# Optimization experiments

Hardware: AMD Instinct MI355X
Metric: run time of the kernel (lower is better)

The kernel has to match this reference:

```python
import jax, jax.numpy as jnp
import numpy as np

NUM_HEADS = 8
DIM = 256
NUM_Q = 1


def setup_inputs() -> dict:
    key = jax.random.key(0)
    ks = jax.random.split(key, 10)
    B, H, W, C = 4, 56, 56, DIM
    mask_h = mask_w = 7
    WinNum = mask_h * mask_w
    x = jax.random.normal(ks[0], (B, H, W, C), dtype=jnp.float32)
    clstoken = jax.random.normal(ks[1], (B, NUM_Q, C), dtype=jnp.float32)
    mask = jax.random.bernoulli(ks[2], 0.3, (B, WinNum, WinNum))
    # ensure each window attends to itself (avoid fully-masked rows)
    eye = jnp.eye(WinNum, dtype=bool)[None]
    mask = jnp.logical_or(mask, eye)
    Wqkv = jax.random.normal(ks[3], (C, 3 * C), dtype=jnp.float32) * (C ** -0.5)
    bqkv = jnp.zeros((3 * C,), dtype=jnp.float32)
    Wo = jax.random.normal(ks[4], (C, C), dtype=jnp.float32) * (C ** -0.5)
    bo = jnp.zeros((C,), dtype=jnp.float32)
    lepe_k = jax.random.normal(ks[5], (3, 3, 1, C), dtype=jnp.float32) * 0.1  # depthwise HWIO
    lepe_b = jnp.zeros((C,), dtype=jnp.float32)
    return {"x": x, "clstoken": clstoken, "mask": mask, "mask_h": mask_h,
            "mask_w": mask_w, "Wqkv": Wqkv, "bqkv": bqkv, "Wo": Wo, "bo": bo,
            "lepe_k": lepe_k, "lepe_b": lepe_b}


def _forward(x, clstoken, mask, mask_h, mask_w, Wqkv, bqkv, Wo, bo, lepe_k, lepe_b):
    B, H, W, C = x.shape
    num_q = clstoken.shape[1]
    Nh = NUM_HEADS
    Hd = C // Nh
    Win_h, Win_w = H // mask_h, W // mask_w
    WinPix = Win_h * Win_w
    WinNum = mask_h * mask_w
    L_win = H * W
    scale = C ** -0.5

    qkv = x @ Wqkv + bqkv                       # [B,H,W,3C]
    q, k, v = jnp.split(qkv, 3, axis=-1)
    qkv_cls = clstoken @ Wqkv + bqkv            # [B,Q,3C]
    q_cls, k_cls, v_cls = jnp.split(qkv_cls, 3, axis=-1)

    # depthwise lepe conv on v (NHWC)
    lepe = jax.lax.conv_general_dilated(
        v, lepe_k, window_strides=(1, 1), padding='SAME',
        dimension_numbers=('NHWC', 'HWIO', 'NHWC'), feature_group_count=C) + lepe_b

    def to_win(t):  # b (j h)(i w)(Nh Hd) -> b Nh (j i h w) Hd
        t = t.reshape(B, mask_h, Win_h, mask_w, Win_w, Nh, Hd)
        t = t.transpose(0, 5, 1, 3, 2, 4, 6)
        return t.reshape(B, Nh, L_win, Hd)

    def cls_heads(t):  # b q (Nh Hd) -> b Nh q Hd
        return t.reshape(B, num_q, Nh, Hd).transpose(0, 2, 1, 3)

    q_all = jnp.concatenate([to_win(q), cls_heads(q_cls)], axis=2)
    k_all = jnp.concatenate([to_win(k), cls_heads(k_cls)], axis=2)
    v_all = jnp.concatenate([to_win(v), cls_heads(v_cls)], axis=2)

    # token-level block mask; cls block (id WinNum) is globally visible
    blk = jnp.concatenate([jnp.arange(L_win) // WinPix,
                           jnp.full((num_q,), WinNum)])
    mask_ext = jnp.pad(mask, ((0, 0), (0, 1), (0, 1)), constant_values=True)
    tok_mask = mask_ext[:, blk[:, None], blk[None, :]]  # [B,L,L]

    scores = jnp.einsum('bnqd,bnkd->bnqk', q_all, k_all) * scale
    neg = jnp.finfo(scores.dtype).min
    scores = jnp.where(tok_mask[:, None], scores, neg)
    attn = jax.nn.softmax(scores, axis=-1)
    out = jnp.einsum('bnqk,bnkd->bnqd', attn, v_all)   # [B,Nh,L,Hd]

    cls_out = out[:, :, -num_q:, :]
    x_out = out[:, :, :-num_q, :]
    # b Nh (j i h w) Hd -> b (j h)(i w)(Nh Hd)
    x_out = x_out.reshape(B, Nh, mask_h, mask_w, Win_h, Win_w, Hd)
    x_out = x_out.transpose(0, 2, 4, 3, 5, 1, 6).reshape(B, H, W, C)
    cls_out = cls_out.transpose(0, 2, 1, 3).reshape(B, num_q, C)

    x_out = (x_out + lepe) @ Wo + bo
    cls_out = cls_out @ Wo + bo
    return x_out, cls_out


def reference(x, clstoken, mask, mask_h, mask_w, Wqkv, bqkv, Wo, bo, lepe_k, lepe_b):
    return _forward(x, clstoken, mask, mask_h, mask_w, Wqkv, bqkv, Wo, bo, lepe_k, lepe_b)
```

## Files before the change

kernel.cpp:

```cpp
#include <hip/hip_runtime.h>
#include <math.h>

#define B_      4
#define NH      8
#define HD      32
#define WINNUM  49
#define LWIN    3136
#define NTOK    3137
#define NPIX    12544
#define MROWS   12548
#define SCALE_L2E 0.09016844005556021f

typedef _Float16 half_t;
using half8  = __attribute__((ext_vector_type(8))) half_t;
using half4  = __attribute__((ext_vector_type(4))) half_t;
using f32x4  = __attribute__((ext_vector_type(4))) float;
using f32x16 = __attribute__((ext_vector_type(16))) float;

__device__ __forceinline__ float fexp2(float x) {
    return __builtin_amdgcn_exp2f(x);
}
__device__ __forceinline__ unsigned pack2(float a, float b) {
    auto h = __builtin_amdgcn_cvt_pkrtz(a, b);
    return __builtin_bit_cast(unsigned, h);
}
__device__ __forceinline__ half8 as_h8(int4 v) {
    return __builtin_bit_cast(half8, v);
}
__device__ __forceinline__ unsigned short h2u(half_t h) {
    return __builtin_bit_cast(unsigned short, h);
}

__global__ __launch_bounds__(256)
void prep(const float* __restrict__ Wqkv, const float* __restrict__ Wo,
          half_t* __restrict__ Wqkvt, half_t* __restrict__ Wot)
{
    const int idx = blockIdx.x * 256 + threadIdx.x;
    const int stride = gridDim.x * 256;
    for (int i = idx; i < 768 * 256; i += stride) {
        int n = i >> 8, k = i & 255;
        Wqkvt[i] = (half_t)Wqkv[k * 768 + n];
    }
    for (int i = idx; i < 256 * 256; i += stride) {
        int n = i >> 8, k = i & 255;
        Wot[i] = (half_t)Wo[k * 256 + n];
    }
}

__global__ __launch_bounds__(256, 1)
void qkv_gemm(const float* __restrict__ x, const float* __restrict__ cls,
              const half_t* __restrict__ Bt, const float* __restrict__ bqkv,
              half_t* __restrict__ qh, half_t* __restrict__ kh,
              half_t* __restrict__ khcls, half_t* __restrict__ vh,
              half_t* __restrict__ vplain)
{
    __shared__ __align__(16) char smem[40960];
    short (*As)[128 * 40] = (short (*)[128 * 40])smem;
    short (*Bs)[128 * 40] = (short (*)[128 * 40])(smem + 20480);
    half_t* Cl = (half_t*)smem;

    const int m0 = blockIdx.y * 128, n0 = blockIdx.x * 128;
    const int tid = threadIdx.x;
    const int lane = tid & 63, wv = tid >> 6;
    const int wm = wv >> 1, wn = wv & 1;
    const int qi = lane & 15, g = lane >> 4;
    f32x4 acc[4][4] = {};

    float4 rfa[2][2];
    int4 rb[2];
    auto issue = [&](int k0) {
#pragma unroll
        for (int i = 0; i < 2; ++i) {
            int ch = tid + 256 * i;
            int row = ch >> 2, kc = (ch & 3) * 8;
            int m = m0 + row;
            if (m < MROWS) {
                const float* src = ((m < NPIX) ? (x + (size_t)m * 256)
                                               : (cls + (size_t)(m - NPIX) * 256)) + k0 + kc;
                rfa[i][0] = *(const float4*)src;
                rfa[i][1] = *(const float4*)(src + 4);
            } else {
                rfa[i][0] = rfa[i][1] = make_float4(0.f, 0.f, 0.f, 0.f);
            }
            rb[i] = *(const int4*)(Bt + (size_t)(n0 + row) * 256 + k0 + kc);
        }
    };
    auto commit = [&](int bu) {
#pragma unroll
        for (int i = 0; i < 2; ++i) {
            int ch = tid + 256 * i;
            int row = ch >> 2, kc = (ch & 3) * 8;
            uint4 pa = make_uint4(pack2(rfa[i][0].x, rfa[i][0].y), pack2(rfa[i][0].z, rfa[i][0].w),
                                  pack2(rfa[i][1].x, rfa[i][1].y), pack2(rfa[i][1].z, rfa[i][1].w));
            *(uint4*)&As[bu][row * 40 + kc] = pa;
            *(int4*)&Bs[bu][row * 40 + kc] = rb[i];
        }
    };

    issue(0); commit(0);
    __syncthreads();
    int buf = 0;
    for (int s = 0; s < 8; ++s) {
        if (s < 7) issue((s + 1) * 32);
        half8 af[4], bf[4];
#pragma unroll
        for (int f = 0; f < 4; ++f) {
            af[f] = *(const half8*)&As[buf][(wm * 64 + f * 16 + qi) * 40 + g * 8];
            bf[f] = *(const half8*)&Bs[buf][(wn * 64 + f * 16 + qi) * 40 + g * 8];
        }
#pragma unroll
        for (int fm = 0; fm < 4; ++fm)
#pragma unroll
            for (int fn = 0; fn < 4; ++fn)
                acc[fm][fn] = __builtin_amdgcn_mfma_f32_16x16x32_f16(af[fm], bf[fn], acc[fm][fn], 0, 0, 0);
        if (s < 7) commit(buf ^ 1);
        __syncthreads();
        buf ^= 1;
    }

    const int part = n0 >> 8;
    const int headbase = (n0 & 255) >> 5;

    float bq[4];
#pragma unroll
    for (int fn = 0; fn < 4; ++fn) bq[fn] = bqkv[n0 + wn * 64 + fn * 16 + qi];
#pragma unroll
    for (int fm = 0; fm < 4; ++fm)
#pragma unroll
        for (int r = 0; r < 4; ++r) {
            int rl = wm * 64 + fm * 16 + g * 4 + r;
#pragma unroll
            for (int fn = 0; fn < 4; ++fn) {
                float val = acc[fm][fn][r] + bq[fn];
                if (part == 0) val *= SCALE_L2E;
                Cl[rl * 136 + wn * 64 + fn * 16 + qi] = (half_t)val;
            }
        }
    __syncthreads();

    if (part == 0 || part == 2) {
        half_t* base = (part == 0) ? qh : vplain;
#pragma unroll
        for (int c = 0; c < 2; ++c) {
            int ch = tid + 256 * c;
            int row = ch >> 2, hd4 = ch & 3;
            int m = m0 + row;
            if (m >= MROWS) continue;
            int b, tok;
            if (m < NPIX) {
                b = m / LWIN;
                int p = m - b * LWIN;
                int hh = p / 56, ww = p - hh * 56;
                tok = ((hh >> 3) * 7 + (ww >> 3)) * 64 + ((hh & 7) << 3) + (ww & 7);
            } else { b = m - NPIX; tok = LWIN; }
            size_t bh = (size_t)(b * NH + headbase + hd4);
            const half_t* src = Cl + row * 136 + hd4 * 32;
            half_t* dst = base + (bh * NTOK + tok) * 32;
#pragma unroll
            for (int j = 0; j < 4; ++j)
                *(int4*)(dst + j * 8) = *(const int4*)(src + j * 8);
        }
    }
    if (part == 1) {
#pragma unroll
        for (int c = 0; c < 2; ++c) {
            int ch = tid + 256 * c;
            int row = ch >> 2, hd4 = ch & 3;
            int m = m0 + row;
            if (m >= MROWS) continue;
            size_t bh;
            half_t* dst;
            if (m < NPIX) {
                int b = m / LWIN;
                int p = m - b * LWIN;
                int hh = p / 56, ww = p - hh * 56;
                int tok = ((hh >> 3) * 7 + (ww >> 3)) * 64 + ((hh & 7) << 3) + (ww & 7);
                bh = (size_t)(b * NH + headbase + hd4);
                dst = kh + bh * (WINNUM * 2560) + (tok >> 6) * 2560 + (tok & 63) * 40;
            } else {
                bh = (size_t)((m - NPIX) * NH + headbase + hd4);
                dst = khcls + bh * 32;
            }
            const half_t* src = Cl + row * 136 + hd4 * 32;
#pragma unroll
            for (int j = 0; j < 4; ++j)
                *(int4*)(dst + j * 8) = *(const int4*)(src + j * 8);
        }
    }
    if (part == 2) {
#pragma unroll
        for (int c = 0; c < 8; ++c) {
            int ch = tid + 256 * c;
            int run = ch >> 7;
            int hd4 = (ch >> 5) & 3;
            int d   = ch & 31;
            int m = m0 + run * 8;
            if (m >= NPIX) continue;
            int b = m / LWIN;
            int p = m - b * LWIN;
            int hh = p / 56, ww = p - hh * 56;
            int win = (hh >> 3) * 7 + (ww >> 3);
            int tokb = (hh & 7) << 3;
            const half_t* src = Cl + (run * 8) * 136 + hd4 * 32 + d;
            unsigned w0 = (unsigned)h2u(src[0])       | ((unsigned)h2u(src[136]) << 16);
            unsigned w1 = (unsigned)h2u(src[2 * 136]) | ((unsigned)h2u(src[3 * 136]) << 16);
            unsigned w2 = (unsigned)h2u(src[4 * 136]) | ((unsigned)h2u(src[5 * 136]) << 16);
            unsigned w3 = (unsigned)h2u(src[6 * 136]) | ((unsigned)h2u(src[7 * 136]) << 16);
            size_t bh = (size_t)(b * NH + headbase + hd4);
            half_t* dst = vh + bh * (WINNUM * 2560) + win * 2560 + d * 80 + tokb;
            *(int4*)dst = make_int4(w0, w1, w2, w3);
        }
    }
}

__global__ __launch_bounds__(128, 1)
void win_attn(const half_t* __restrict__ qh, const half_t* __restrict__ kh,
              const half_t* __restrict__ khcls, const half_t* __restrict__ vh,
              const half_t* __restrict__ vplain, const int* __restrict__ mask,
              const float* __restrict__ lk, const float* __restrict__ lb,
              half_t* __restrict__ tg, float* __restrict__ clspart,
              half_t* __restrict__ t2)
{
    const int id = blockIdx.x;
    const int tid = threadIdx.x;
    __shared__ __align__(16) short Plds[2][32 * 72];
    __shared__ float redc[2 * 33];
    const int lane = tid & 63, wv = tid >> 6;

    if (id >= 1824) {
        for (int task = (id - 1824) * 128 + tid; task < NPIX * 32; task += 784 * 128) {
            const int pix = task >> 5, cg = task & 31;
            const int c0 = cg * 8;
            const int b = pix / LWIN, p = pix - b * LWIN;
            const int hh = p / 56, ww = p - hh * 56;
            const int nh = c0 >> 5, d0 = c0 & 31;
            const half_t* vb = vplain + (size_t)(b * NH + nh) * NTOK * 32 + d0;
            float s[8];
#pragma unroll
            for (int j = 0; j < 8; ++j) s[j] = lb[c0 + j];
#pragma unroll
            for (int dh = -1; dh <= 1; ++dh) {
                int hn = hh + dh;
                if (hn < 0 || hn >= 56) continue;
#pragma unroll
                for (int dw = -1; dw <= 1; ++dw) {
                    int wn = ww + dw;
                    if (wn < 0 || wn >= 56) continue;
                    int tok = ((hn >> 3) * 7 + (wn >> 3)) * 64 + ((hn & 7) << 3) + (wn & 7);
                    half8 vvv = *(const half8*)(vb + (size_t)tok * 32);
                    const float* kk = lk + ((dh + 1) * 3 + (dw + 1)) * 256 + c0;
#pragma unroll
                    for (int j = 0; j < 8; ++j) s[j] += (float)vvv[j] * kk[j];
                }
            }
            half8 outv;
#pragma unroll
            for (int j = 0; j < 8; ++j) outv[j] = (half_t)s[j];
            *(half8*)(t2 + (size_t)pix * 256 + c0) = outv;
        }
        return;
    }

    if (id >= 1568) {
        const int cid = id - 1568;
        const int bh = cid >> 3;
        const int chunk = cid & 7;
        const int wstart = chunk * 6;
        const int nw = (chunk < 7) ? 6 : 7;
        const int nkeys = nw * 64;

        float q[32];
        {
            const half_t* qp = qh + ((size_t)bh * NTOK + LWIN) * 32;
#pragma unroll
            for (int d = 0; d < 32; ++d) q[d] = (float)qp[d];
        }
        float l = 0.f, o[32];
#pragma unroll
        for (int d = 0; d < 32; ++d) o[d] = 0.f;

        const half_t* kwb = kh + (size_t)bh * (WINNUM * 2560) + wstart * 2560;
        const half_t* vb  = vplain + ((size_t)bh * NTOK + wstart * 64) * 32;

        for (int kk = tid; kk < nkeys; kk += 128) {
            const half_t* kp = kwb + (kk >> 6) * 2560 + (kk & 63) * 40;
            float s = 0.f;
#pragma unroll
            for (int c8 = 0; c8 < 4; ++c8) {
                half8 kv = *(const half8*)(kp + c8 * 8);
#pragma unroll
                for (int j = 0; j < 8; ++j) s += q[c8 * 8 + j] * (float)kv[j];
            }
            float pp = fexp2(s);
            l += pp;
            const half_t* vp = vb + (size_t)kk * 32;
#pragma unroll
            for (int c8 = 0; c8 < 4; ++c8) {
                half8 vvv = *(const half8*)(vp + c8 * 8);
#pragma unroll
                for (int j = 0; j < 8; ++j) o[c8 * 8 + j] += pp * (float)vvv[j];
            }
        }
        if (chunk == 7 && tid == 0) {
            const half_t* kp = khcls + bh * 32;
            float s = 0.f;
#pragma unroll
            for (int d = 0; d < 32; ++d) s += q[d] * (float)kp[d];
            float pp = fexp2(s);
            l += pp;
            const half_t* vp = vplain + ((size_t)bh * NTOK + LWIN) * 32;
#pragma unroll
            for (int d = 0; d < 32; ++d) o[d] += pp * (float)vp[d];
        }
#pragma unroll
        for (int off = 1; off < 64; off <<= 1) {
            l += __shfl_xor(l, off);
#pragma unroll
            for (int d = 0; d < 32; ++d) o[d] += __shfl_xor(o[d], off);
        }
        if (lane == 0) {
#pragma unroll
            for (int d = 0; d < 32; ++d) redc[wv * 33 + d] = o[d];
            redc[wv * 33 + 32] = l;
        }
        __syncthreads();
        if (tid < 33) {
            clspart[(bh * 8 + chunk) * 33 + tid] = redc[tid] + redc[33 + tid];
        }
        return;
    }

    const int sw = (id & 7) * 196 + (id >> 3);
    const int wi = sw % 49;
    const int bh = sw / 49;
    const int b = bh >> 3, nh = bh & 7;

    const int qc = lane & 31;
    const int hb = lane >> 5;
    const int qbase = wi * 64 + wv * 32;

    const half_t* qp = qh + ((size_t)bh * NTOK + qbase + qc) * 32 + hb * 8;
    half8 aq0 = as_h8(*(const int4*)(qp));
    half8 aq1 = as_h8(*(const int4*)(qp + 16));

    const f32x16 Z16 = {0.f,0.f,0.f,0.f,0.f,0.f,0.f,0.f,0.f,0.f,0.f,0.f,0.f,0.f,0.f,0.f};
    f32x16 acc = Z16;
    float lacc = 0.f;

    const int* mrow = mask + (b * WINNUM + wi) * WINNUM;
    int mv = (lane < WINNUM) ? mrow[lane] : 0;
    unsigned long long rem = __ballot(mv != 0);

    const half_t* kwin = kh + (size_t)bh * (WINNUM * 2560);
    const half_t* vwin = vh + (size_t)bh * (WINNUM * 2560);

    short* pw = &Plds[wv][qc * 72];
    const short* prd = &Plds[wv][qc * 72 + hb * 8];

    while (rem) {
        const int wj = __builtin_ctzll(rem);
        rem &= rem - 1;
        const half_t* kb = kwin + wj * 2560 + qc * 40 + hb * 8;
        const half_t* vb = vwin + wj * 2560 + qc * 80 + hb * 8;
        int4 kf00 = *(const int4*)(kb);
        int4 kf01 = *(const int4*)(kb + 16);
        int4 kf10 = *(const int4*)(kb + 1280);
        int4 kf11 = *(const int4*)(kb + 1296);
        int4 vf0 = *(const int4*)(vb);
        int4 vf1 = *(const int4*)(vb + 16);
        int4 vf2 = *(const int4*)(vb + 32);
        int4 vf3 = *(const int4*)(vb + 48);

        f32x16 st0, st1;
        __builtin_amdgcn_s_setprio(1);
        st0 = __builtin_amdgcn_mfma_f32_32x32x16_f16(as_h8(kf00), aq0, Z16, 0, 0, 0);
        st1 = __builtin_amdgcn_mfma_f32_32x32x16_f16(as_h8(kf10), aq0, Z16, 0, 0, 0);
        st0 = __builtin_amdgcn_mfma_f32_32x32x16_f16(as_h8(kf01), aq1, st0, 0, 0, 0);
        st1 = __builtin_amdgcn_mfma_f32_32x32x16_f16(as_h8(kf11), aq1, st1, 0, 0, 0);
        __builtin_amdgcn_s_setprio(0);

#pragma unroll
        for (int rb = 0; rb < 4; ++rb) {
            float p0 = fexp2(st0[4 * rb + 0]);
            float p1 = fexp2(st0[4 * rb + 1]);
            float p2 = fexp2(st0[4 * rb + 2]);
            float p3 = fexp2(st0[4 * rb + 3]);
            lacc += (p0 + p1) + (p2 + p3);
            *(uint2*)&pw[8 * rb + 4 * hb] = make_uint2(pack2(p0, p1), pack2(p2, p3));
        }
#pragma unroll
        for (int rb = 0; rb < 4; ++rb) {
            float p0 = fexp2(st1[4 * rb + 0]);
            float p1 = fexp2(st1[4 * rb + 1]);
            float p2 = fexp2(st1[4 * rb + 2]);
            float p3 = fexp2(st1[4 * rb + 3]);
            lacc += (p0 + p1) + (p2 + p3);
            *(uint2*)&pw[32 + 8 * rb + 4 * hb] = make_uint2(pack2(p0, p1), pack2(p2, p3));
        }
        half8 pB0 = *(const half8*)(prd);
        half8 pB1 = *(const half8*)(prd + 16);
        half8 pB2 = *(const half8*)(prd + 32);
        half8 pB3 = *(const half8*)(prd + 48);
        __builtin_amdgcn_s_setprio(1);
        acc = __builtin_amdgcn_mfma_f32_32x32x16_f16(as_h8(vf0), pB0, acc, 0, 0, 0);
        acc = __builtin_amdgcn_mfma_f32_32x32x16_f16(as_h8(vf1), pB1, acc, 0, 0, 0);
        acc = __builtin_amdgcn_mfma_f32_32x32x16_f16(as_h8(vf2), pB2, acc, 0, 0, 0);
        acc = __builtin_amdgcn_mfma_f32_32x32x16_f16(as_h8(vf3), pB3, acc, 0, 0, 0);
        __builtin_amdgcn_s_setprio(0);
    }

    lacc += __shfl_xor(lacc, 32);

    float sc = 0.f;
    {
        const half_t* kcb = khcls + bh * 32 + hb * 8;
        half8 kc0 = *(const half8*)(kcb);
        half8 kc1 = *(const half8*)(kcb + 16);
#pragma unroll
        for (int j = 0; j < 8; ++j)
            sc += (float)aq0[j] * (float)kc0[j] + (float)aq1[j] * (float)kc1[j];
        sc += __shfl_xor(sc, 32);
    }
    float pc = fexp2(sc);
    float l = lacc + pc;
    {
        const half_t* vcb = vplain + ((size_t)bh * NTOK + LWIN) * 32;
#pragma unroll
        for (int rb = 0; rb < 4; ++rb) {
            half4 vc = *(const half4*)(vcb + 8 * rb + 4 * hb);
#pragma unroll
            for (int r = 0; r < 4; ++r) acc[4 * rb + r] += pc * (float)vc[r];
        }
    }

    {
        float inv = 1.f / l;
        int kk = wv * 32 + qc;
        int hh = (wi / 7) * 8 + (kk >> 3);
        int ww = (wi % 7) * 8 + (kk & 7);
        size_t pix = (size_t)b * LWIN + hh * 56 + ww;
        half_t* tp = tg + pix * 256 + nh * 32;
#pragma unroll
        for (int rb = 0; rb < 4; ++rb) {
            half4 hv;
#pragma unroll
            for (int r = 0; r < 4; ++r) hv[r] = (half_t)(acc[4 * rb + r] * inv);
            *(half4*)(tp + 8 * rb + 4 * hb) = hv;
        }
    }
}

__global__ __launch_bounds__(256, 1)
void out_gemm(const half_t* __restrict__ th, const half_t* __restrict__ t2,
              const float* __restrict__ clspart,
              const half_t* __restrict__ Bt, const float* __restrict__ bo,
              float* __restrict__ out)
{
    __shared__ __align__(16) short As[2][64 * 40];
    __shared__ __align__(16) short Bs[2][128 * 40];
    const int m0 = blockIdx.y * 64, n0 = blockIdx.x * 128;
    const int tid = threadIdx.x;
    const int lane = tid & 63, wv = tid >> 6;
    const int wm = wv >> 1, wn = wv & 1;
    const int qi = lane & 15, g = lane >> 4;
    f32x4 acc[2][4] = {};

    int4 ra, rb[2];
    auto issue = [&](int k0) {
        {
            int row = tid >> 2, kc = (tid & 3) * 8;
            int m = m0 + row;
            if (m < NPIX) {
                half8 a = *(const half8*)(th + (size_t)m * 256 + k0 + kc);
                half8 b2 = *(const half8*)(t2 + (size_t)m * 256 + k0 + kc);
                half8 s = a + b2;
                ra = __builtin_bit_cast(int4, s);
            } else if (m < MROWS) {
                int bcls = m - NPIX;
                half_t tmp[8];
#pragma unroll
                for (int j = 0; j < 8; ++j) {
                    int c = k0 + kc + j;
                    int bh = bcls * NH + (c >> 5);
                    int d = c & 31;
                    float os = 0.f, ls = 0.f;
#pragma unroll
                    for (int ch = 0; ch < 8; ++ch) {
                        os += clspart[(bh * 8 + ch) * 33 + d];
                        ls += clspart[(bh * 8 + ch) * 33 + 32];
                    }
                    tmp[j] = (half_t)(os / ls);
                }
                ra = *(const int4*)tmp;
            } else {
                ra = make_int4(0, 0, 0, 0);
            }
        }
#pragma unroll
        for (int i = 0; i < 2; ++i) {
            int ch = tid + 256 * i;
            int row = ch >> 2, kc = (ch & 3) * 8;
            rb[i] = *(const int4*)(Bt + (size_t)(n0 + row) * 256 + k0 + kc);
        }
    };
    auto commit = [&](int bu) {
        {
            int row = tid >> 2, kc = (tid & 3) * 8;
            *(int4*)&As[bu][row * 40 + kc] = ra;
        }
#pragma unroll
        for (int i = 0; i < 2; ++i) {
            int ch = tid + 256 * i;
            int row = ch >> 2, kc = (ch & 3) * 8;
            *(int4*)&Bs[bu][row * 40 + kc] = rb[i];
        }
    };

    issue(0); commit(0);
    __syncthreads();
    int buf = 0;
    for (int s = 0; s < 8; ++s) {
        if (s < 7) issue((s + 1) * 32);
        half8 af[2], bf[4];
#pragma unroll
        for (int f = 0; f < 2; ++f)
            af[f] = *(const half8*)&As[buf][(wm * 32 + f * 16 + qi) * 40 + g * 8];
#pragma unroll
        for (int f = 0; f < 4; ++f)
            bf[f] = *(const half8*)&Bs[buf][(wn * 64 + f * 16 + qi) * 40 + g * 8];
#pragma unroll
        for (int fm = 0; fm < 2; ++fm)
#pragma unroll
            for (int fn = 0; fn < 4; ++fn)
                acc[fm][fn] = __builtin_amdgcn_mfma_f32_16x16x32_f16(af[fm], bf[fn], acc[fm][fn], 0, 0, 0);
        if (s < 7) commit(buf ^ 1);
        __syncthreads();
        buf ^= 1;
    }

    float bov[4];
    int nn[4];
#pragma unroll
    for (int fn = 0; fn < 4; ++fn) {
        nn[fn] = n0 + wn * 64 + fn * 16 + qi;
        bov[fn] = bo[nn[fn]];
    }
#pragma unroll
    for (int fm = 0; fm < 2; ++fm)
#pragma unroll
        for (int r = 0; r < 4; ++r) {
            int m = m0 + wm * 32 + fm * 16 + g * 4 + r;
            if (m >= MROWS) continue;
#pragma unroll
            for (int fn = 0; fn < 4; ++fn)
                out[(size_t)m * 256 + nn[fn]] = acc[fm][fn][r] + bov[fn];
        }
}

extern "C" void kernel_launch(void* const* d_in, const int* in_sizes, int n_in,
                              void* d_out, int out_size, void* d_ws, size_t ws_size,
                              hipStream_t stream)
{
    const float* x    = (const float*)d_in[0];
    const float* cls  = (const float*)d_in[1];
    const int*   mask = (const int*)d_in[2];
    const float* Wqkv = (const float*)d_in[5];
    const float* bqkv = (const float*)d_in[6];
    const float* Wo   = (const float*)d_in[7];
    const float* bo   = (const float*)d_in[8];
    const float* lk   = (const float*)d_in[9];
    const float* lb   = (const float*)d_in[10];
    float* out = (float*)d_out;

    char* w = (char*)d_ws;
    half_t* qh     = (half_t*)w;  w += 6424576;
    half_t* kh     = (half_t*)w;  w += 8028160;
    half_t* khcls  = (half_t*)w;  w += 2048;
    half_t* vh     = (half_t*)w;  w += 8028160;
    half_t* vplain = (half_t*)w;  w += 6424576;
    half_t* Wqkvt  = (half_t*)w;  w += 393216;
    half_t* Wot    = (half_t*)w;  w += 131072;
    half_t* th     = (half_t*)w;  w += 6424576;
    half_t* t2     = (half_t*)w;  w += 6424576;
    float*  clspart= (float*)w;   w += 33792;

    prep<<<256, 256, 0, stream>>>(Wqkv, Wo, Wqkvt, Wot);
    qkv_gemm<<<dim3(6, 99), 256, 0, stream>>>(x, cls, Wqkvt, bqkv, qh, kh, khcls, vh, vplain);
    win_attn<<<2608, 128, 0, stream>>>(qh, kh, khcls, vh, vplain, mask, lk, lb, th, clspart, t2);
    out_gemm<<<dim3(2, 197), 256, 0, stream>>>(th, t2, clspart, Wot, bo, out);
}
```

Before: 103.1 us.

## Widen QKV GEMM tile to 128x256 with 512 threads

The QKV projection GEMM now uses 512-thread blocks that each compute a 128x256 output tile, covering a full q/k/v part per block. This halves the number of blocks and the number of times each fp32 x row is loaded and converted to half. The epilogue is split into two phases through the same LDS staging buffer, one per half of the heads. The trade-offs are a larger LDS footprint, an extra barrier phase, and 297 blocks, which may leave the 256 CUs unevenly loaded.

Measured after the change: 107.1 us. 1.04x slower.

```diff
diff --git a/kernel.cpp b/kernel.cpp
--- a/kernel.cpp
+++ b/kernel.cpp
@@ -47,52 +47,60 @@
     }
 }
 
-__global__ __launch_bounds__(256, 1)
+__global__ __launch_bounds__(512, 1)
 void qkv_gemm(const float* __restrict__ x, const float* __restrict__ cls,
               const half_t* __restrict__ Bt, const float* __restrict__ bqkv,
               half_t* __restrict__ qh, half_t* __restrict__ kh,
               half_t* __restrict__ khcls, half_t* __restrict__ vh,
               half_t* __restrict__ vplain)
 {
-    __shared__ __align__(16) char smem[40960];
+    __shared__ __align__(16) char smem[61440];
     short (*As)[128 * 40] = (short (*)[128 * 40])smem;
-    short (*Bs)[128 * 40] = (short (*)[128 * 40])(smem + 20480);
+    short (*Bs)[256 * 40] = (short (*)[256 * 40])(smem + 20480);
     half_t* Cl = (half_t*)smem;
 
-    const int m0 = blockIdx.y * 128, n0 = blockIdx.x * 128;
+    const int m0 = blockIdx.y * 128;
+    const int part = blockIdx.x;
+    const int n0 = part * 256;
     const int tid = threadIdx.x;
     const int lane = tid & 63, wv = tid >> 6;
-    const int wm = wv >> 1, wn = wv & 1;
+    const int wm = wv >> 2, wn = wv & 3;
     const int qi = lane & 15, g = lane >> 4;
     f32x4 acc[4][4] = {};
 
-    float4 rfa[2][2];
+    float4 rfa[2];
     int4 rb[2];
     auto issue = [&](int k0) {
-#pragma unroll
-        for (int i = 0; i < 2; ++i) {
-            int ch = tid + 256 * i;
-            int row = ch >> 2, kc = (ch & 3) * 8;
+        {
+            int row = tid >> 2, kc = (tid & 3) * 8;
             int m = m0 + row;
             if (m < MROWS) {
                 const float* src = ((m < NPIX) ? (x + (size_t)m * 256)
                                                : (cls + (size_t)(m - NPIX) * 256)) + k0 + kc;
-                rfa[i][0] = *(const float4*)src;
-                rfa[i][1] = *(const float4*)(src + 4);
+                rfa[0] = *(const float4*)src;
+                rfa[1] = *(const float4*)(src + 4);
             } else {
-                rfa[i][0] = rfa[i][1] = make_float4(0.f, 0.f, 0.f, 0.f);
-            }
+                rfa[0] = rfa[1] = make_float4(0.f, 0.f, 0.f, 0.f);
+            }
+        }
+#pragma unroll
+        for (int i = 0; i < 2; ++i) {
+            int ch = tid + 512 * i;
+            int row = ch >> 2, kc = (ch & 3) * 8;
             rb[i] = *(const int4*)(Bt + (size_t)(n0 + row) * 256 + k0 + kc);
         }
     };
     auto commit = [&](int bu) {
+        {
+            int row = tid >> 2, kc = (tid & 3) * 8;
+            uint4 pa = make_uint4(pack2(rfa[0].x, rfa[0].y), pack2(rfa[0].z, rfa[0].w),
+                                  pack2(rfa[1].x, rfa[1].y), pack2(rfa[1].z, rfa[1].w));
+            *(uint4*)&As[bu][row * 40 + kc] = pa;
+        }
 #pragma unroll
         for (int i = 0; i < 2; ++i) {
-            int ch = tid + 256 * i;
+            int ch = tid + 512 * i;
             int row = ch >> 2, kc = (ch & 3) * 8;
-            uint4 pa = make_uint4(pack2(rfa[i][0].x, rfa[i][0].y), pack2(rfa[i][0].z, rfa[i][0].w),
-                                  pack2(rfa[i][1].x, rfa[i][1].y), pack2(rfa[i][1].z, rfa[i][1].w));
-            *(uint4*)&As[bu][row * 40 + kc] = pa;
             *(int4*)&Bs[bu][row * 40 + kc] = rb[i];
         }
     };
@@ -118,97 +126,95 @@
         buf ^= 1;
     }
 
-    const int part = n0 >> 8;
-    const int headbase = (n0 & 255) >> 5;
-
     float bq[4];
 #pragma unroll
     for (int fn = 0; fn < 4; ++fn) bq[fn] = bqkv[n0 + wn * 64 + fn * 16 + qi];
-#pragma unroll
-    for (int fm = 0; fm < 4; ++fm)
-#pragma unroll
-        for (int r = 0; r < 4; ++r) {
-            int rl = wm * 64 + fm * 16 + g * 4 + r;
-#pragma unroll
-            for (int fn = 0; fn < 4; ++fn) {
-                float val = acc[fm][fn][r] + bq[fn];
-                if (part == 0) val *= SCALE_L2E;
-                Cl[rl * 136 + wn * 64 + fn * 16 + qi] = (half_t)val;
-            }
-        }
-    __syncthreads();
-
-    if (part == 0 || part == 2) {
-        half_t* base = (part == 0) ? qh : vplain;
-#pragma unroll
-        for (int c = 0; c < 2; ++c) {
-            int ch = tid + 256 * c;
-            int row = ch >> 2, hd4 = ch & 3;
+
+#pragma unroll
+    for (int ph = 0; ph < 2; ++ph) {
+        __syncthreads();
+        if ((wn >> 1) == ph) {
+#pragma unroll
+            for (int fm = 0; fm < 4; ++fm)
+#pragma unroll
+                for (int r = 0; r < 4; ++r) {
+                    int rl = wm * 64 + fm * 16 + g * 4 + r;
+#pragma unroll
+                    for (int fn = 0; fn < 4; ++fn) {
+                        float val = acc[fm][fn][r] + bq[fn];
+                        if (part == 0) val *= SCALE_L2E;
+                        Cl[rl * 136 + (wn & 1) * 64 + fn * 16 + qi] = (half_t)val;
+                    }
+                }
+        }
+        __syncthreads();
+
+        if (part == 0 || part == 2) {
+            half_t* base = (part == 0) ? qh : vplain;
+            int row = tid >> 2, hd4 = tid & 3;
             int m = m0 + row;
-            if (m >= MROWS) continue;
-            int b, tok;
-            if (m < NPIX) {
-                b = m / LWIN;
-                int p = m - b * LWIN;
-                int hh = p / 56, ww = p - hh * 56;
-                tok = ((hh >> 3) * 7 + (ww >> 3)) * 64 + ((hh & 7) << 3) + (ww & 7);
-            } else { b = m - NPIX; tok = LWIN; }
-            size_t bh = (size_t)(b * NH + headbase + hd4);
-            const half_t* src = Cl + row * 136 + hd4 * 32;
-            half_t* dst = base + (bh * NTOK + tok) * 32;
-#pragma unroll
-            for (int j = 0; j < 4; ++j)
-                *(int4*)(dst + j * 8) = *(const int4*)(src + j * 8);
-        }
-    }
-    if (part == 1) {
-#pragma unroll
-        for (int c = 0; c < 2; ++c) {
-            int ch = tid + 256 * c;
-            int row = ch >> 2, hd4 = ch & 3;
+            if (m < MROWS) {
+                int b, tok;
+                if (m < NPIX) {
+                    b = m / LWIN;
+                    int p = m - b * LWIN;
+                    int hh = p / 56, ww = p - hh * 56;
+                    tok = ((hh >> 3) * 7 + (ww >> 3)) * 64 + ((hh & 7) << 3) + (ww & 7);
+                } else { b = m - NPIX; tok = LWIN; }
+                size_t bh = (size_t)(b * NH + ph * 4 + hd4);
+                const half_t* src = Cl + row * 136 + hd4 * 32;
+                half_t* dst = base + (bh * NTOK + tok) * 32;
+#pragma unroll
+                for (int j = 0; j < 4; ++j)
+                    *(int4*)(dst + j * 8) = *(const int4*)(src + j * 8);
+            }
+        }
+        if (part == 1) {
+            int row = tid >> 2, hd4 = tid & 3;
             int m = m0 + row;
-            if (m >= MROWS) continue;
-            size_t bh;
-            half_t* dst;
-            if (m < NPIX) {
+            if (m < MROWS) {
+                size_t bh;
+                half_t* dst;
+                if (m < NPIX) {
+                    int b = m / LWIN;
+                    int p = m - b * LWIN;
+                    int hh = p / 56, ww = p - hh * 56;
+                    int tok = ((hh >> 3) * 7 + (ww >> 3)) * 64 + ((hh & 7) << 3) + (ww & 7);
+                    bh = (size_t)(b * NH + ph * 4 + hd4);
+                    dst = kh + bh * (WINNUM * 2560) + (tok >> 6) * 2560 + (tok & 63) * 40;
+                } else {
+                    bh = (size_t)((m - NPIX) * NH + ph * 4 + hd4);
+                    dst = khcls + bh * 32;
+                }
+                const half_t* src = Cl + row * 136 + hd4 * 32;
+#pragma unroll
+                for (int j = 0; j < 4; ++j)
+                    *(int4*)(dst + j * 8) = *(const int4*)(src + j * 8);
+            }
+        }
+        if (part == 2) {
+#pragma unroll
+            for (int c = 0; c < 4; ++c) {
+                int ch = tid + 512 * c;
+                int run = ch >> 7;
+                int hd4 = (ch >> 5) & 3;
+                int d   = ch & 31;
+                int m = m0 + run * 8;
+                if (m >= NPIX) continue;
                 int b = m / LWIN;
                 int p = m - b * LWIN;
                 int hh = p / 56, ww = p - hh * 56;
-                int tok = ((hh >> 3) * 7 + (ww >> 3)) * 64 + ((hh & 7) << 3) + (ww & 7);
-                bh = (size_t)(b * NH + headbase + hd4);
-                dst = kh + bh * (WINNUM * 2560) + (tok >> 6) * 2560 + (tok & 63) * 40;
-            } else {
-                bh = (size_t)((m - NPIX) * NH + headbase + hd4);
-                dst = khcls + bh * 32;
-            }
-            const half_t* src = Cl + row * 136 + hd4 * 32;
-#pragma unroll
-            for (int j = 0; j < 4; ++j)
-                *(int4*)(dst + j * 8) = *(const int4*)(src + j * 8);
-        }
-    }
-    if (part == 2) {
-#pragma unroll
-        for (int c = 0; c < 8; ++c) {
-            int ch = tid + 256 * c;
-            int run = ch >> 7;
-            int hd4 = (ch >> 5) & 3;
-            int d   = ch & 31;
-            int m = m0 + run * 8;
-            if (m >= NPIX) continue;
-            int b = m / LWIN;
-            int p = m - b * LWIN;
-            int hh = p / 56, ww = p - hh * 56;
-            int win = (hh >> 3) * 7 + (ww >> 3);
-            int tokb = (hh & 7) << 3;
-            const half_t* src = Cl + (run * 8) * 136 + hd4 * 32 + d;
-            unsigned w0 = (unsigned)h2u(src[0])       | ((unsigned)h2u(src[136]) << 16);
-            unsigned w1 = (unsigned)h2u(src[2 * 136]) | ((unsigned)h2u(src[3 * 136]) << 16);
-            unsigned w2 = (unsigned)h2u(src[4 * 136]) | ((unsigned)h2u(src[5 * 136]) << 16);
-            unsigned w3 = (unsigned)h2u(src[6 * 136]) | ((unsigned)h2u(src[7 * 136]) << 16);
-            size_t bh = (size_t)(b * NH + headbase + hd4);
-            half_t* dst = vh + bh * (WINNUM * 2560) + win * 2560 + d * 80 + tokb;
-            *(int4*)dst = make_int4(w0, w1, w2, w3);
+                int win = (hh >> 3) * 7 + (ww >> 3);
+                int tokb = (hh & 7) << 3;
+                const half_t* src = Cl + (run * 8) * 136 + hd4 * 32 + d;
+                unsigned w0 = (unsigned)h2u(src[0])       | ((unsigned)h2u(src[136]) << 16);
+                unsigned w1 = (unsigned)h2u(src[2 * 136]) | ((unsigned)h2u(src[3 * 136]) << 16);
+                unsigned w2 = (unsigned)h2u(src[4 * 136]) | ((unsigned)h2u(src[5 * 136]) << 16);
+                unsigned w3 = (unsigned)h2u(src[6 * 136]) | ((unsigned)h2u(src[7 * 136]) << 16);
+                size_t bh = (size_t)(b * NH + ph * 4 + hd4);
+                half_t* dst = vh + bh * (WINNUM * 2560) + win * 2560 + d * 80 + tokb;
+                *(int4*)dst = make_int4(w0, w1, w2, w3);
+            }
         }
     }
 }
@@ -585,7 +591,7 @@
     float*  clspart= (float*)w;   w += 33792;
 
     prep<<<256, 256, 0, stream>>>(Wqkv, Wo, Wqkvt, Wot);
-    qkv_gemm<<<dim3(6, 99), 256, 0, stream>>>(x, cls, Wqkvt, bqkv, qh, kh, khcls, vh, vplain);
+    qkv_gemm<<<dim3(3, 99), 512, 0, stream>>>(x, cls, Wqkvt, bqkv, qh, kh, khcls, vh, vplain);
     win_attn<<<2608, 128, 0, stream>>>(qh, kh, khcls, vh, vplain, mask, lk, lb, th, clspart, t2);
     out_gemm<<<dim3(2, 197), 256, 0, stream>>>(th, t2, clspart, Wot, bo, out);
 }
```

## Split window attention key blocks across two workgroups and merge in output GEMM

Applied to the files above, without the earlier changes.

Each query window's visible key windows are dealt alternately to two workgroups, which doubles the attention grid. Each half writes a partial normalized output and its softmax denominator, and the output GEMM's A-load merges the two halves with denominator weights before adding lepe. The aim is more parallelism and better load balance across CUs in the attention kernel. The cost is extra global traffic from a second output buffer plus denominator arrays, and more work in the GEMM prologue. The softmax has no max-subtraction, so summing the denominators stays consistent.

Result: slower. 107.3 us (+4.0%).

```diff
diff --git a/kernel.cpp b/kernel.cpp
--- a/kernel.cpp
+++ b/kernel.cpp
@@ -218,8 +218,9 @@
               const half_t* __restrict__ khcls, const half_t* __restrict__ vh,
               const half_t* __restrict__ vplain, const int* __restrict__ mask,
               const float* __restrict__ lk, const float* __restrict__ lb,
-              half_t* __restrict__ tg, float* __restrict__ clspart,
-              half_t* __restrict__ t2)
+              half_t* __restrict__ o1, half_t* __restrict__ o2,
+              float* __restrict__ lp1, float* __restrict__ lp2,
+              float* __restrict__ clspart, half_t* __restrict__ t2)
 {
     const int id = blockIdx.x;
     const int tid = threadIdx.x;
@@ -227,8 +228,8 @@
     __shared__ float redc[2 * 33];
     const int lane = tid & 63, wv = tid >> 6;
 
-    if (id >= 1824) {
-        for (int task = (id - 1824) * 128 + tid; task < NPIX * 32; task += 784 * 128) {
+    if (id >= 3392) {
+        for (int task = (id - 3392) * 128 + tid; task < NPIX * 32; task += 784 * 128) {
             const int pix = task >> 5, cg = task & 31;
             const int c0 = cg * 8;
             const int b = pix / LWIN, p = pix - b * LWIN;
@@ -261,8 +262,8 @@
         return;
     }
 
-    if (id >= 1568) {
-        const int cid = id - 1568;
+    if (id >= 3136) {
+        const int cid = id - 3136;
         const int bh = cid >> 3;
         const int chunk = cid & 7;
         const int wstart = chunk * 6;
@@ -330,7 +331,9 @@
         return;
     }
 
-    const int sw = (id & 7) * 196 + (id >> 3);
+    const int par = id & 1;
+    const int sid = id >> 1;
+    const int sw = (sid & 7) * 196 + (sid >> 3);
     const int wi = sw % 49;
     const int bh = sw / 49;
     const int b = bh >> 3, nh = bh & 7;
@@ -349,7 +352,18 @@
 
     const int* mrow = mask + (b * WINNUM + wi) * WINNUM;
     int mv = (lane < WINNUM) ? mrow[lane] : 0;
-    unsigned long long rem = __ballot(mv != 0);
+    unsigned long long all = __ballot(mv != 0);
+    unsigned long long rem = 0;
+    {
+        unsigned long long t = all;
+        int i = 0;
+        while (t) {
+            int j = __builtin_ctzll(t);
+            t &= t - 1;
+            if ((i & 1) == par) rem |= (1ull << j);
+            ++i;
+        }
+    }
 
     const half_t* kwin = kh + (size_t)bh * (WINNUM * 2560);
     const half_t* vwin = vh + (size_t)bh * (WINNUM * 2560);
@@ -411,8 +425,8 @@
 
     lacc += __shfl_xor(lacc, 32);
 
-    float sc = 0.f;
-    {
+    if (par == 0) {
+        float sc = 0.f;
         const half_t* kcb = khcls + bh * 32 + hb * 8;
         half8 kc0 = *(const half8*)(kcb);
         half8 kc1 = *(const half8*)(kcb + 16);
@@ -420,10 +434,8 @@
         for (int j = 0; j < 8; ++j)
             sc += (float)aq0[j] * (float)kc0[j] + (float)aq1[j] * (float)kc1[j];
         sc += __shfl_xor(sc, 32);
-    }
-    float pc = fexp2(sc);
-    float l = lacc + pc;
-    {
+        float pc = fexp2(sc);
+        lacc += pc;
         const half_t* vcb = vplain + ((size_t)bh * NTOK + LWIN) * 32;
 #pragma unroll
         for (int rb = 0; rb < 4; ++rb) {
@@ -434,25 +446,27 @@
     }
 
     {
-        float inv = 1.f / l;
+        float inv = (lacc > 0.f) ? (1.f / lacc) : 0.f;
         int kk = wv * 32 + qc;
         int hh = (wi / 7) * 8 + (kk >> 3);
         int ww = (wi % 7) * 8 + (kk & 7);
         size_t pix = (size_t)b * LWIN + hh * 56 + ww;
-        half_t* tp = tg + pix * 256 + nh * 32;
+        half_t* op = (par == 0 ? o1 : o2) + pix * 256 + nh * 32;
 #pragma unroll
         for (int rb = 0; rb < 4; ++rb) {
             half4 hv;
 #pragma unroll
             for (int r = 0; r < 4; ++r) hv[r] = (half_t)(acc[4 * rb + r] * inv);
-            *(half4*)(tp + 8 * rb + 4 * hb) = hv;
-        }
+            *(half4*)(op + 8 * rb + 4 * hb) = hv;
+        }
+        if (hb == 0) (par == 0 ? lp1 : lp2)[pix * 8 + nh] = lacc;
     }
 }
 
 __global__ __launch_bounds__(256, 1)
-void out_gemm(const half_t* __restrict__ th, const half_t* __restrict__ t2,
-              const float* __restrict__ clspart,
+void out_gemm(const half_t* __restrict__ o1, const half_t* __restrict__ o2,
+              const float* __restrict__ lp1, const float* __restrict__ lp2,
+              const half_t* __restrict__ t2, const float* __restrict__ clspart,
               const half_t* __restrict__ Bt, const float* __restrict__ bo,
               float* __restrict__ out)
 {
@@ -470,17 +484,27 @@
         {
             int row = tid >> 2, kc = (tid & 3) * 8;
             int m = m0 + row;
+            int c0 = k0 + kc;
             if (m < NPIX) {
-                half8 a = *(const half8*)(th + (size_t)m * 256 + k0 + kc);
-                half8 b2 = *(const half8*)(t2 + (size_t)m * 256 + k0 + kc);
-                half8 s = a + b2;
-                ra = __builtin_bit_cast(int4, s);
+                int nh = c0 >> 5;
+                float l1 = lp1[(size_t)m * 8 + nh];
+                float l2 = lp2[(size_t)m * 8 + nh];
+                float rcp = 1.f / (l1 + l2);
+                float w1 = l1 * rcp, w2 = l2 * rcp;
+                half8 a1 = *(const half8*)(o1 + (size_t)m * 256 + c0);
+                half8 a2 = *(const half8*)(o2 + (size_t)m * 256 + c0);
+                half8 bb = *(const half8*)(t2 + (size_t)m * 256 + c0);
+                half_t tmp[8];
+#pragma unroll
+                for (int j = 0; j < 8; ++j)
+                    tmp[j] = (half_t)((float)a1[j] * w1 + (float)a2[j] * w2 + (float)bb[j]);
+                ra = *(const int4*)tmp;
             } else if (m < MROWS) {
                 int bcls = m - NPIX;
                 half_t tmp[8];
 #pragma unroll
                 for (int j = 0; j < 8; ++j) {
-                    int c = k0 + kc + j;
+                    int c = c0 + j;
                     int bh = bcls * NH + (c >> 5);
                     int d = c & 31;
                     float os = 0.f, ls = 0.f;
@@ -580,12 +604,16 @@
     half_t* vplain = (half_t*)w;  w += 6424576;
     half_t* Wqkvt  = (half_t*)w;  w += 393216;
     half_t* Wot    = (half_t*)w;  w += 131072;
-    half_t* th     = (half_t*)w;  w += 6424576;
+    half_t* o1     = (half_t*)w;  w += 6424576;
+    half_t* o2     = (half_t*)w;  w += 6424576;
+    float*  lp1    = (float*)w;   w += 401408;
+    float*  lp2    = (float*)w;   w += 401408;
     half_t* t2     = (half_t*)w;  w += 6424576;
     float*  clspart= (float*)w;   w += 33792;
 
     prep<<<256, 256, 0, stream>>>(Wqkv, Wo, Wqkvt, Wot);
     qkv_gemm<<<dim3(6, 99), 256, 0, stream>>>(x, cls, Wqkvt, bqkv, qh, kh, khcls, vh, vplain);
-    win_attn<<<2608, 128, 0, stream>>>(qh, kh, khcls, vh, vplain, mask, lk, lb, th, clspart, t2);
-    out_gemm<<<dim3(2, 197), 256, 0, stream>>>(th, t2, clspart, Wot, bo, out);
-}
+    win_attn<<<4176, 128, 0, stream>>>(qh, kh, khcls, vh, vplain, mask, lk, lb,
+                                       o1, o2, lp1, lp2, clspart, t2);
+    out_gemm<<<dim3(2, 197), 256, 0, stream>>>(o1, o2, lp1, lp2, t2, clspart, Wot, bo, out);
+}
```
